# Optimization experiments

Hardware: AMD Instinct MI355X
Metric: run time of the kernel (lower is better)

Reference implementation:

```python
import jax, jax.numpy as jnp
import numpy as np


def setup_inputs() -> dict:
    key = jax.random.key(0)
    kq, kk, kv = jax.random.split(key, 3)
    S, D = 8192, 128
    return {
        "Q": jax.random.normal(kq, (S, D), dtype=jnp.float32),
        "K": jax.random.normal(kk, (S, D), dtype=jnp.float32),
        "V": jax.random.normal(kv, (S, D), dtype=jnp.float32),
    }


def reference(Q, K, V):
    d_k = Q.shape[-1]
    scale = 1.0 / jnp.sqrt(jnp.asarray(d_k, Q.dtype))
    scores = (Q @ K.T) * scale          # [S, S]
    attn = jax.nn.softmax(scores, axis=-1)
    return attn @ V                     # [S, Dv]
```

## Files before the change

### kernel.cpp

```cpp
#include <hip/hip_runtime.h>
#include <hip/hip_bf16.h>
#include <hip/hip_fp16.h>
#include <math.h>

typedef __attribute__((ext_vector_type(8))) short short8;
typedef __attribute__((ext_vector_type(16))) float f32x16;
typedef __attribute__((ext_vector_type(4))) unsigned short ushort4v;
typedef __attribute__((ext_vector_type(4))) unsigned int uint4v;

#define S 8192
#define D 128
#define QBLK 128
#define KVB 32

__device__ __forceinline__ unsigned short f2bf(float f) {
    unsigned int x = __float_as_uint(f);
    unsigned int r = x + 0x7fffu + ((x >> 16) & 1u);
    return (unsigned short)(r >> 16);
}

__device__ __forceinline__ unsigned int cvtpk(float a, float b) {
    unsigned int r;
    asm("v_cvt_pk_bf16_f32 %0, %1, %2" : "=v"(r) : "v"(a), "v"(b));
    return r;
}

__device__ __forceinline__ float fexp2(float x) { return __builtin_amdgcn_exp2f(x); }

__device__ __forceinline__ void gl_lds16(const unsigned short* g, unsigned short* l) {
    __builtin_amdgcn_global_load_lds(
        (const __attribute__((address_space(1))) unsigned int*)g,
        (__attribute__((address_space(3))) unsigned int*)l, 16, 0, 0);
}

__device__ __forceinline__ void plswap(unsigned int& a, unsigned int& b, int hi) {
#if __has_builtin(__builtin_amdgcn_permlane32_swap)
    auto r = __builtin_amdgcn_permlane32_swap((int)a, (int)b, false, false);
    a = (unsigned int)r[0];
    b = (unsigned int)r[1];
#else
    unsigned int xa = (unsigned int)__shfl_xor((int)a, 32, 64);
    unsigned int xb = (unsigned int)__shfl_xor((int)b, 32, 64);
    unsigned int na = hi ? xb : a;
    unsigned int nb = hi ? b : xa;
    a = na; b = nb;
#endif
}

union W4 { unsigned int u[4]; short8 v; };

__global__ __launch_bounds__(256) void prep_kv(const float* __restrict__ K,
                                               const float* __restrict__ V,
                                               unsigned short* __restrict__ Kb,
                                               unsigned short* __restrict__ Vt) {
    __shared__ unsigned short T[64][72];
    const float scale = 0.12751743022854459f;
    int s0 = blockIdx.x * 64, d0 = blockIdx.y * 64;
    int tr = threadIdx.x >> 4, tc = (threadIdx.x & 15) * 4;
#pragma unroll
    for (int p = 0; p < 4; ++p) {
        int r = p * 16 + tr;
        float4 kf = *reinterpret_cast<const float4*>(K + (size_t)(s0 + r) * D + d0 + tc);
        ushort4v ko = { f2bf(kf.x * scale), f2bf(kf.y * scale),
                        f2bf(kf.z * scale), f2bf(kf.w * scale) };
        *reinterpret_cast<ushort4v*>(Kb + (size_t)(s0 + r) * D + d0 + tc) = ko;
        float4 v = *reinterpret_cast<const float4*>(V + (size_t)(s0 + r) * D + d0 + tc);
        ushort4v vo = { f2bf(v.x), f2bf(v.y), f2bf(v.z), f2bf(v.w) };
        *reinterpret_cast<ushort4v*>(&T[r][tc]) = vo;
    }
    __syncthreads();
#pragma unroll
    for (int p = 0; p < 4; ++p) {
        int dr = p * 16 + tr;
        ushort4v o = { T[tc + 0][dr], T[tc + 1][dr], T[tc + 2][dr], T[tc + 3][dr] };
        *reinterpret_cast<ushort4v*>(Vt + (size_t)(d0 + dr) * S + s0 + tc) = o;
    }
}

#define QKOP(acc, kc) (acc) = __builtin_amdgcn_mfma_f32_32x32x16_bf16(              \
    *reinterpret_cast<const short8*>(                                               \
        &Kl[(size_t)c31 * 128 + (((2 * (kc) + hi) ^ (c31 & 15)) * 8)]),             \
    qf[kc], (acc), 0, 0, 0)

#define PVOP(oo, pp, dt, off) (oo) = __builtin_amdgcn_mfma_f32_32x32x16_bf16(       \
    (pp).v,                                                                          \
    *reinterpret_cast<const short8*>(                                               \
        &Vl[((dt) * 32 + c31) * 32 + ((((off) + hi) ^ sw) * 8)]),                    \
    (oo), 0, 0, 0)

#define SMEXG(g)                                                                     \
    {                                                                                \
        float e0 = fexp2(sa[4 * (g) + 0] + sb[4 * (g) + 0]);                         \
        float e1 = fexp2(sa[4 * (g) + 1] + sb[4 * (g) + 1]);                         \
        float e2 = fexp2(sa[4 * (g) + 2] + sb[4 * (g) + 2]);                         \
        float e3 = fexp2(sa[4 * (g) + 3] + sb[4 * (g) + 3]);                         \
        l_r += (e0 + e1) + (e2 + e3);                                                \
        wd[2 * (g) + 0] = cvtpk(e0, e1);                                             \
        wd[2 * (g) + 1] = cvtpk(e2, e3);                                             \
    }

#define SMFIN(PD0, PD1)                                                              \
    {                                                                                \
        plswap(wd[0], wd[2], hi); plswap(wd[1], wd[3], hi);                          \
        plswap(wd[4], wd[6], hi); plswap(wd[5], wd[7], hi);                          \
        PD0.u[0] = wd[0]; PD0.u[1] = wd[1]; PD0.u[2] = wd[2]; PD0.u[3] = wd[3];      \
        PD1.u[0] = wd[4]; PD1.u[1] = wd[5]; PD1.u[2] = wd[6]; PD1.u[3] = wd[7];      \
    }

#define STAGE_K(RING) do {                                                           \
    gl_lds16(kg[0], &Klds[RING][(w * 2 + 0) * 512]); kg[0] += (size_t)KVB * D;       \
    gl_lds16(kg[1], &Klds[RING][(w * 2 + 1) * 512]); kg[1] += (size_t)KVB * D;       \
} while (0)

#define STAGE_V(RING) do {                                                           \
    gl_lds16(vg[0], &Vlds[RING][(w * 2 + 0) * 512]); vg[0] += KVB;                   \
    gl_lds16(vg[1], &Vlds[RING][(w * 2 + 1) * 512]); vg[1] += KVB;                   \
} while (0)

#define PHASE_BARRIER() do {                                                         \
    asm volatile("s_waitcnt vmcnt(0)" ::: "memory");                                 \
    __builtin_amdgcn_s_barrier();                                                    \
    __builtin_amdgcn_sched_barrier(0);                                               \
} while (0)

#define SUBTILE(KR, VR, PP0, PP1, QQ0, QQ1)                                          \
    {                                                                                \
        const unsigned short* Kl = Klds[KR];                                         \
        const unsigned short* Vl = Vlds[VR];                                         \
        f32x16 sa, sb;                                                               \
        _Pragma("unroll")                                                            \
        for (int i = 0; i < 16; ++i) { sa[i] = 0.f; sb[i] = 0.f; }                   \
        __builtin_amdgcn_s_setprio(1);                                               \
        QKOP(sa, 0); QKOP(sb, 1); QKOP(sa, 2); QKOP(sb, 3);                          \
        QKOP(sa, 4); QKOP(sb, 5); QKOP(sa, 6); QKOP(sb, 7);                          \
        __builtin_amdgcn_s_setprio(0);                                               \
        unsigned int wd[8];                                                          \
        PVOP(o0, PP0, 0, 0); PVOP(o0, PP1, 0, 2);                                    \
        SMEXG(0);                                                                    \
        PVOP(o1, PP0, 1, 0); PVOP(o1, PP1, 1, 2);                                    \
        SMEXG(1);                                                                    \
        PVOP(o2, PP0, 2, 0); PVOP(o2, PP1, 2, 2);                                    \
        SMEXG(2);                                                                    \
        PVOP(o3, PP0, 3, 0); PVOP(o3, PP1, 3, 2);                                    \
        SMEXG(3);                                                                    \
        SMFIN(QQ0, QQ1);                                                             \
    }

#define SUBTILE_NOPV(KR, QQ0, QQ1)                                                   \
    {                                                                                \
        const unsigned short* Kl = Klds[KR];                                         \
        f32x16 sa, sb;                                                               \
        _Pragma("unroll")                                                            \
        for (int i = 0; i < 16; ++i) { sa[i] = 0.f; sb[i] = 0.f; }                   \
        __builtin_amdgcn_s_setprio(1);                                               \
        QKOP(sa, 0); QKOP(sb, 1); QKOP(sa, 2); QKOP(sb, 3);                          \
        QKOP(sa, 4); QKOP(sb, 5); QKOP(sa, 6); QKOP(sb, 7);                          \
        __builtin_amdgcn_s_setprio(0);                                               \
        unsigned int wd[8];                                                          \
        SMEXG(0); SMEXG(1); SMEXG(2); SMEXG(3);                                      \
        SMFIN(QQ0, QQ1);                                                             \
    }

__global__ __launch_bounds__(256, 2) void attn_fwd(
    const float* __restrict__ Q, const unsigned short* __restrict__ Kb,
    const unsigned short* __restrict__ Vtg, float* __restrict__ out,
    __half* __restrict__ wsO, float* __restrict__ wsL, int split)
{
    __shared__ __attribute__((aligned(16))) unsigned short Klds[4][KVB * D];
    __shared__ __attribute__((aligned(16))) unsigned short Vlds[4][D * KVB];

    const int tid  = threadIdx.x;
    const int w    = tid >> 6;
    const int lane = tid & 63;
    const int hi   = lane >> 5;
    const int c31  = lane & 31;
    const int sw   = (c31 >> 1) & 3;
    const int bid  = blockIdx.x;
    const int sp   = bid % split;
    const int qb   = bid / split;
    const int chunk  = S / split;
    const int kv0    = sp * chunk;
    const int ntiles = chunk / KVB;

    short8 qf[8];
    {
        const float* qrow = Q + (size_t)(qb * QBLK + w * 32 + c31) * D;
#pragma unroll
        for (int kc = 0; kc < 8; ++kc) {
            float4 x = *reinterpret_cast<const float4*>(qrow + kc * 16 + hi * 8);
            float4 y = *reinterpret_cast<const float4*>(qrow + kc * 16 + hi * 8 + 4);
            W4 u;
            u.u[0] = cvtpk(x.x, x.y); u.u[1] = cvtpk(x.z, x.w);
            u.u[2] = cvtpk(y.x, y.y); u.u[3] = cvtpk(y.z, y.w);
            qf[kc] = u.v;
        }
    }

    const unsigned short* kg[2];
    const unsigned short* vg[2];
#pragma unroll
    for (int i = 0; i < 2; ++i) {
        int krow = w * 8 + i * 4 + (lane >> 4);
        int kch  = (lane & 15) ^ (krow & 15);
        kg[i] = Kb + (size_t)(kv0 + krow) * D + kch * 8;
        int vrow = w * 32 + i * 16 + (lane >> 2);
        int vch  = (lane & 3) ^ ((vrow >> 1) & 3);
        vg[i] = Vtg + (size_t)vrow * S + kv0 + vch * 8;
    }

    f32x16 o0, o1, o2, o3;
#pragma unroll
    for (int i = 0; i < 16; ++i) { o0[i] = 0.f; o1[i] = 0.f; o2[i] = 0.f; o3[i] = 0.f; }
    float l_r = 0.f;
    W4 pX0, pX1, pY0, pY1;

    STAGE_K(0); STAGE_K(1); STAGE_V(0);

    PHASE_BARRIER();
    STAGE_K(2); STAGE_K(3);
    STAGE_V(1); STAGE_V(2);
    SUBTILE_NOPV(0, pY0, pY1);
    SUBTILE(1, 0, pY0, pY1, pX0, pX1);

    const int npair = ntiles / 4 - 1;
#pragma unroll 1
    for (int j = 0; j < npair; ++j) {
        PHASE_BARRIER();
        STAGE_K(0); STAGE_K(1);
        STAGE_V(3); STAGE_V(0);
        SUBTILE(2, 1, pX0, pX1, pY0, pY1);
        SUBTILE(3, 2, pY0, pY1, pX0, pX1);
        PHASE_BARRIER();
        STAGE_K(2); STAGE_K(3);
        STAGE_V(1); STAGE_V(2);
        SUBTILE(0, 3, pX0, pX1, pY0, pY1);
        SUBTILE(1, 0, pY0, pY1, pX0, pX1);
    }

    PHASE_BARRIER();
    STAGE_V(3);
    SUBTILE(2, 1, pX0, pX1, pY0, pY1);
    SUBTILE(3, 2, pY0, pY1, pX0, pX1);

    PHASE_BARRIER();
    {
        const unsigned short* Vl = Vlds[3];
        __builtin_amdgcn_s_setprio(1);
        PVOP(o0, pX0, 0, 0); PVOP(o0, pX1, 0, 2);
        PVOP(o1, pX0, 1, 0); PVOP(o1, pX1, 1, 2);
        PVOP(o2, pX0, 2, 0); PVOP(o2, pX1, 2, 2);
        PVOP(o3, pX0, 3, 0); PVOP(o3, pX1, 3, 2);
        __builtin_amdgcn_s_setprio(0);
    }

    float l_tot = l_r + __shfl_xor(l_r, 32, 64);
    if (split == 1) {
#pragma unroll
        for (int reg = 0; reg < 16; ++reg) {
            int crow = (reg & 3) + 8 * (reg >> 2) + 4 * hi;
            float lr  = __shfl(l_tot, crow, 64);
            float inv = 1.f / lr;
            size_t rb = (size_t)(qb * QBLK + w * 32 + crow) * D;
            out[rb +  0 + c31] = o0[reg] * inv;
            out[rb + 32 + c31] = o1[reg] * inv;
            out[rb + 64 + c31] = o2[reg] * inv;
            out[rb + 96 + c31] = o3[reg] * inv;
        }
    } else {
        __half* Opart = wsO + (size_t)(qb * split + sp) * (QBLK * D);
#pragma unroll
        for (int reg = 0; reg < 16; ++reg) {
            int crow = (reg & 3) + 8 * (reg >> 2) + 4 * hi;
            size_t rb = (size_t)(w * 32 + crow) * D;
            Opart[rb +  0 + c31] = __float2half(o0[reg]);
            Opart[rb + 32 + c31] = __float2half(o1[reg]);
            Opart[rb + 64 + c31] = __float2half(o2[reg]);
            Opart[rb + 96 + c31] = __float2half(o3[reg]);
        }
        if (hi == 0)
            wsL[(size_t)(qb * split + sp) * QBLK + w * 32 + c31] = l_tot;
    }
}

__global__ void attn_combine(const __half* __restrict__ wsO,
                             const float* __restrict__ wsL,
                             float* __restrict__ out, int split)
{
    int idx = blockIdx.x * blockDim.x + threadIdx.x;
    if (idx >= S * D / 8) return;
    int row = idx >> 4;
    int g   = (idx & 15) * 8;
    int qb = row >> 7, rloc = row & 127;
    float acc[8];
#pragma unroll
    for (int i = 0; i < 8; ++i) acc[i] = 0.f;
    float L = 0.f;
    for (int s = 0; s < split; ++s) {
        size_t b = (size_t)(qb * split + s);
        const __half* p = wsO + b * (QBLK * D) + (size_t)rloc * D + g;
        uint4v u = *reinterpret_cast<const uint4v*>(p);
#pragma unroll
        for (int i = 0; i < 4; ++i) {
            unsigned int wbits = u[i];
            __half2 h = *reinterpret_cast<__half2*>(&wbits);
            float2 f = __half22float2(h);
            acc[2 * i]     += f.x;
            acc[2 * i + 1] += f.y;
        }
        L += wsL[b * QBLK + rloc];
    }
    float inv = 1.f / L;
    size_t ob = (size_t)row * D + g;
    float4 w0 = { acc[0] * inv, acc[1] * inv, acc[2] * inv, acc[3] * inv };
    float4 w1 = { acc[4] * inv, acc[5] * inv, acc[6] * inv, acc[7] * inv };
    *reinterpret_cast<float4*>(out + ob)     = w0;
    *reinterpret_cast<float4*>(out + ob + 4) = w1;
}

extern "C" void kernel_launch(void* const* d_in, const int* in_sizes, int n_in,
                              void* d_out, int out_size, void* d_ws, size_t ws_size,
                              hipStream_t stream) {
    const float* Q = (const float*)d_in[0];
    const float* K = (const float*)d_in[1];
    const float* V = (const float*)d_in[2];
    float* out = (float*)d_out;

    size_t base = 2ull * S * D * sizeof(unsigned short);
    int split = 1;
    for (int sp = 8; sp >= 2; sp >>= 1) {
        size_t need = base + (size_t)sp * S * D * sizeof(__half)
                    + (size_t)sp * S * sizeof(float);
        if (ws_size >= need) { split = sp; break; }
    }

    unsigned short* Kb = (unsigned short*)d_ws;
    unsigned short* Vt = Kb + (size_t)S * D;
    __half* wsO = (__half*)(Vt + (size_t)S * D);
    float* wsL = (float*)(wsO + (size_t)split * S * D);

    prep_kv<<<dim3(S / 64, D / 64), 256, 0, stream>>>(K, V, Kb, Vt);
    attn_fwd<<<(S / QBLK) * split, 256, 0, stream>>>(Q, Kb, Vt, out, wsO, wsL, split);
    if (split > 1)
        attn_combine<<<(S * D / 8 + 255) / 256, 256, 0, stream>>>(wsO, wsL, out, split);
}
```

Before: 56.86 us.

## Pre-swizzle V into MFMA fragment layout and load it directly to registers

The prep kernel now writes V into a layout that matches the MFMA B-operand fragment order. The attention kernel loads each tile's V fragments straight from global memory into registers, which removes the V shared-memory ring, its staging and its LDS reads. The QK accumulation is merged into a single accumulator instead of two interleaved ones. The allowed split count rises to 16. This cuts LDS traffic and LDS footprint, which may help occupancy, but it exposes global-load latency inside the loop and adds register pressure from holding eight V fragments.

```diff
diff --git a/kernel.cpp b/kernel.cpp
--- a/kernel.cpp
+++ b/kernel.cpp
@@ -52,7 +52,7 @@
 __global__ __launch_bounds__(256) void prep_kv(const float* __restrict__ K,
                                                const float* __restrict__ V,
                                                unsigned short* __restrict__ Kb,
-                                               unsigned short* __restrict__ Vt) {
+                                               unsigned short* __restrict__ Vf) {
     __shared__ unsigned short T[64][72];
     const float scale = 0.12751743022854459f;
     int s0 = blockIdx.x * 64, d0 = blockIdx.y * 64;
@@ -72,8 +72,16 @@
 #pragma unroll
     for (int p = 0; p < 4; ++p) {
         int dr = p * 16 + tr;
+        int d  = d0 + dr;
+        int s  = s0 + tc;
+        int t  = s >> 5;
+        int ks = (s >> 3) & 3;
+        int dt = d >> 5;
+        int lane2 = (d & 31) | ((ks & 1) << 5);
+        int f = dt * 2 + (ks >> 1);
+        size_t idx = (((size_t)t * 8 + f) * 64 + lane2) * 8 + (s & 7);
         ushort4v o = { T[tc + 0][dr], T[tc + 1][dr], T[tc + 2][dr], T[tc + 3][dr] };
-        *reinterpret_cast<ushort4v*>(Vt + (size_t)(d0 + dr) * S + s0 + tc) = o;
+        *reinterpret_cast<ushort4v*>(Vf + idx) = o;
     }
 }
 
@@ -82,18 +90,22 @@
         &Kl[(size_t)c31 * 128 + (((2 * (kc) + hi) ^ (c31 & 15)) * 8)]),             \
     qf[kc], (acc), 0, 0, 0)
 
-#define PVOP(oo, pp, dt, off) (oo) = __builtin_amdgcn_mfma_f32_32x32x16_bf16(       \
-    (pp).v,                                                                          \
-    *reinterpret_cast<const short8*>(                                               \
-        &Vl[((dt) * 32 + c31) * 32 + ((((off) + hi) ^ sw) * 8)]),                    \
-    (oo), 0, 0, 0)
+#define PVOPR(oo, pp, dt, off) (oo) = __builtin_amdgcn_mfma_f32_32x32x16_bf16(      \
+    (pp).v, vr[(dt) * 2 + (off) / 2], (oo), 0, 0, 0)
+
+#define LOADV do {                                                                   \
+    _Pragma("unroll")                                                                \
+    for (int f_ = 0; f_ < 8; ++f_)                                                   \
+        vr[f_] = *reinterpret_cast<const short8*>(vfp + f_ * 512);                   \
+    vfp += 4096;                                                                     \
+} while (0)
 
 #define SMEXG(g)                                                                     \
     {                                                                                \
-        float e0 = fexp2(sa[4 * (g) + 0] + sb[4 * (g) + 0]);                         \
-        float e1 = fexp2(sa[4 * (g) + 1] + sb[4 * (g) + 1]);                         \
-        float e2 = fexp2(sa[4 * (g) + 2] + sb[4 * (g) + 2]);                         \
-        float e3 = fexp2(sa[4 * (g) + 3] + sb[4 * (g) + 3]);                         \
+        float e0 = fexp2(s[4 * (g) + 0]);                                            \
+        float e1 = fexp2(s[4 * (g) + 1]);                                            \
+        float e2 = fexp2(s[4 * (g) + 2]);                                            \
+        float e3 = fexp2(s[4 * (g) + 3]);                                            \
         l_r += (e0 + e1) + (e2 + e3);                                                \
         wd[2 * (g) + 0] = cvtpk(e0, e1);                                             \
         wd[2 * (g) + 1] = cvtpk(e2, e3);                                             \
@@ -112,50 +124,42 @@
     gl_lds16(kg[1], &Klds[RING][(w * 2 + 1) * 512]); kg[1] += (size_t)KVB * D;       \
 } while (0)
 
-#define STAGE_V(RING) do {                                                           \
-    gl_lds16(vg[0], &Vlds[RING][(w * 2 + 0) * 512]); vg[0] += KVB;                   \
-    gl_lds16(vg[1], &Vlds[RING][(w * 2 + 1) * 512]); vg[1] += KVB;                   \
-} while (0)
-
 #define PHASE_BARRIER() do {                                                         \
     asm volatile("s_waitcnt vmcnt(0)" ::: "memory");                                 \
     __builtin_amdgcn_s_barrier();                                                    \
     __builtin_amdgcn_sched_barrier(0);                                               \
 } while (0)
 
-#define SUBTILE(KR, VR, PP0, PP1, QQ0, QQ1)                                          \
+#define SUBTILE(KR, PP0, PP1, QQ0, QQ1)                                              \
     {                                                                                \
         const unsigned short* Kl = Klds[KR];                                         \
-        const unsigned short* Vl = Vlds[VR];                                         \
-        f32x16 sa, sb;                                                               \
+        f32x16 s;                                                                    \
         _Pragma("unroll")                                                            \
-        for (int i = 0; i < 16; ++i) { sa[i] = 0.f; sb[i] = 0.f; }                   \
+        for (int i = 0; i < 16; ++i) s[i] = 0.f;                                     \
         __builtin_amdgcn_s_setprio(1);                                               \
-        QKOP(sa, 0); QKOP(sb, 1); QKOP(sa, 2); QKOP(sb, 3);                          \
-        QKOP(sa, 4); QKOP(sb, 5); QKOP(sa, 6); QKOP(sb, 7);                          \
+        QKOP(s, 0); QKOP(s, 1); QKOP(s, 2); QKOP(s, 3);                              \
+        QKOP(s, 4); QKOP(s, 5); QKOP(s, 6); QKOP(s, 7);                              \
         __builtin_amdgcn_s_setprio(0);                                               \
         unsigned int wd[8];                                                          \
-        PVOP(o0, PP0, 0, 0); PVOP(o0, PP1, 0, 2);                                    \
-        SMEXG(0);                                                                    \
-        PVOP(o1, PP0, 1, 0); PVOP(o1, PP1, 1, 2);                                    \
-        SMEXG(1);                                                                    \
-        PVOP(o2, PP0, 2, 0); PVOP(o2, PP1, 2, 2);                                    \
-        SMEXG(2);                                                                    \
-        PVOP(o3, PP0, 3, 0); PVOP(o3, PP1, 3, 2);                                    \
-        SMEXG(3);                                                                    \
+        PVOPR(o0, PP0, 0, 0); PVOPR(o0, PP1, 0, 2); SMEXG(0);                        \
+        PVOPR(o1, PP0, 1, 0); PVOPR(o1, PP1, 1, 2); SMEXG(1);                        \
+        PVOPR(o2, PP0, 2, 0); PVOPR(o2, PP1, 2, 2); SMEXG(2);                        \
+        PVOPR(o3, PP0, 3, 0); PVOPR(o3, PP1, 3, 2); SMEXG(3);                        \
+        LOADV;                                                                       \
         SMFIN(QQ0, QQ1);                                                             \
     }
 
 #define SUBTILE_NOPV(KR, QQ0, QQ1)                                                   \
     {                                                                                \
         const unsigned short* Kl = Klds[KR];                                         \
-        f32x16 sa, sb;                                                               \
+        f32x16 s;                                                                    \
         _Pragma("unroll")                                                            \
-        for (int i = 0; i < 16; ++i) { sa[i] = 0.f; sb[i] = 0.f; }                   \
+        for (int i = 0; i < 16; ++i) s[i] = 0.f;                                     \
         __builtin_amdgcn_s_setprio(1);                                               \
-        QKOP(sa, 0); QKOP(sb, 1); QKOP(sa, 2); QKOP(sb, 3);                          \
-        QKOP(sa, 4); QKOP(sb, 5); QKOP(sa, 6); QKOP(sb, 7);                          \
+        QKOP(s, 0); QKOP(s, 1); QKOP(s, 2); QKOP(s, 3);                              \
+        QKOP(s, 4); QKOP(s, 5); QKOP(s, 6); QKOP(s, 7);                              \
         __builtin_amdgcn_s_setprio(0);                                               \
+        LOADV;                                                                       \
         unsigned int wd[8];                                                          \
         SMEXG(0); SMEXG(1); SMEXG(2); SMEXG(3);                                      \
         SMFIN(QQ0, QQ1);                                                             \
@@ -163,18 +167,16 @@
 
 __global__ __launch_bounds__(256, 2) void attn_fwd(
     const float* __restrict__ Q, const unsigned short* __restrict__ Kb,
-    const unsigned short* __restrict__ Vtg, float* __restrict__ out,
+    const unsigned short* __restrict__ Vf, float* __restrict__ out,
     __half* __restrict__ wsO, float* __restrict__ wsL, int split)
 {
     __shared__ __attribute__((aligned(16))) unsigned short Klds[4][KVB * D];
-    __shared__ __attribute__((aligned(16))) unsigned short Vlds[4][D * KVB];
 
     const int tid  = threadIdx.x;
     const int w    = tid >> 6;
     const int lane = tid & 63;
     const int hi   = lane >> 5;
     const int c31  = lane & 31;
-    const int sw   = (c31 >> 1) & 3;
     const int bid  = blockIdx.x;
     const int sp   = bid % split;
     const int qb   = bid / split;
@@ -197,16 +199,15 @@
     }
 
     const unsigned short* kg[2];
-    const unsigned short* vg[2];
 #pragma unroll
     for (int i = 0; i < 2; ++i) {
         int krow = w * 8 + i * 4 + (lane >> 4);
         int kch  = (lane & 15) ^ (krow & 15);
         kg[i] = Kb + (size_t)(kv0 + krow) * D + kch * 8;
-        int vrow = w * 32 + i * 16 + (lane >> 2);
-        int vch  = (lane & 3) ^ ((vrow >> 1) & 3);
-        vg[i] = Vtg + (size_t)vrow * S + kv0 + vch * 8;
-    }
+    }
+
+    const unsigned short* vfp = Vf + (size_t)(kv0 >> 5) * 4096 + (size_t)lane * 8;
+    short8 vr[8];
 
     f32x16 o0, o1, o2, o3;
 #pragma unroll
@@ -214,42 +215,36 @@
     float l_r = 0.f;
     W4 pX0, pX1, pY0, pY1;
 
-    STAGE_K(0); STAGE_K(1); STAGE_V(0);
+    STAGE_K(0); STAGE_K(1);
 
     PHASE_BARRIER();
     STAGE_K(2); STAGE_K(3);
-    STAGE_V(1); STAGE_V(2);
     SUBTILE_NOPV(0, pY0, pY1);
-    SUBTILE(1, 0, pY0, pY1, pX0, pX1);
+    SUBTILE(1, pY0, pY1, pX0, pX1);
 
     const int npair = ntiles / 4 - 1;
 #pragma unroll 1
     for (int j = 0; j < npair; ++j) {
         PHASE_BARRIER();
         STAGE_K(0); STAGE_K(1);
-        STAGE_V(3); STAGE_V(0);
-        SUBTILE(2, 1, pX0, pX1, pY0, pY1);
-        SUBTILE(3, 2, pY0, pY1, pX0, pX1);
+        SUBTILE(2, pX0, pX1, pY0, pY1);
+        SUBTILE(3, pY0, pY1, pX0, pX1);
         PHASE_BARRIER();
         STAGE_K(2); STAGE_K(3);
-        STAGE_V(1); STAGE_V(2);
-        SUBTILE(0, 3, pX0, pX1, pY0, pY1);
-        SUBTILE(1, 0, pY0, pY1, pX0, pX1);
+        SUBTILE(0, pX0, pX1, pY0, pY1);
+        SUBTILE(1, pY0, pY1, pX0, pX1);
     }
 
     PHASE_BARRIER();
-    STAGE_V(3);
-    SUBTILE(2, 1, pX0, pX1, pY0, pY1);
-    SUBTILE(3, 2, pY0, pY1, pX0, pX1);
-
-    PHASE_BARRIER();
+    SUBTILE(2, pX0, pX1, pY0, pY1);
+    SUBTILE(3, pY0, pY1, pX0, pX1);
+
     {
-        const unsigned short* Vl = Vlds[3];
         __builtin_amdgcn_s_setprio(1);
-        PVOP(o0, pX0, 0, 0); PVOP(o0, pX1, 0, 2);
-        PVOP(o1, pX0, 1, 0); PVOP(o1, pX1, 1, 2);
-        PVOP(o2, pX0, 2, 0); PVOP(o2, pX1, 2, 2);
-        PVOP(o3, pX0, 3, 0); PVOP(o3, pX1, 3, 2);
+        PVOPR(o0, pX0, 0, 0); PVOPR(o0, pX1, 0, 2);
+        PVOPR(o1, pX0, 1, 0); PVOPR(o1, pX1, 1, 2);
+        PVOPR(o2, pX0, 2, 0); PVOPR(o2, pX1, 2, 2);
+        PVOPR(o3, pX0, 3, 0); PVOPR(o3, pX1, 3, 2);
         __builtin_amdgcn_s_setprio(0);
     }
 
@@ -327,19 +322,19 @@
 
     size_t base = 2ull * S * D * sizeof(unsigned short);
     int split = 1;
-    for (int sp = 8; sp >= 2; sp >>= 1) {
+    for (int sp = 16; sp >= 2; sp >>= 1) {
         size_t need = base + (size_t)sp * S * D * sizeof(__half)
                     + (size_t)sp * S * sizeof(float);
         if (ws_size >= need) { split = sp; break; }
     }
 
     unsigned short* Kb = (unsigned short*)d_ws;
-    unsigned short* Vt = Kb + (size_t)S * D;
-    __half* wsO = (__half*)(Vt + (size_t)S * D);
+    unsigned short* Vf = Kb + (size_t)S * D;
+    __half* wsO = (__half*)(Vf + (size_t)S * D);
     float* wsL = (float*)(wsO + (size_t)split * S * D);
 
-    prep_kv<<<dim3(S / 64, D / 64), 256, 0, stream>>>(K, V, Kb, Vt);
-    attn_fwd<<<(S / QBLK) * split, 256, 0, stream>>>(Q, Kb, Vt, out, wsO, wsL, split);
+    prep_kv<<<dim3(S / 64, D / 64), 256, 0, stream>>>(K, V, Kb, Vf);
+    attn_fwd<<<(S / QBLK) * split, 256, 0, stream>>>(Q, Kb, Vf, out, wsO, wsL, split);
     if (split > 1)
         attn_combine<<<(S * D / 8 + 255) / 256, 256, 0, stream>>>(wsO, wsL, out, split);
 }
```

Result: slower. 61.43 us (+8.0%).

## Shrink LDS ring to three slots with mid-phase barrier and allow split 16

Applied to the files above, without the earlier changes.

Replaces the four-slot K/V LDS ring with a three-slot rotating ring, adding a mid-phase barrier so each subtile stages only one K and one V tile ahead. This cuts LDS use per block, which may let more blocks fit per CU. The KV split factor cap also rises from 8 to 16, giving more parallel blocks at the cost of a heavier combine pass and more workspace traffic. The extra barrier adds synchronisation per subtile.

```diff
diff --git a/kernel.cpp b/kernel.cpp
--- a/kernel.cpp
+++ b/kernel.cpp
@@ -12,6 +12,7 @@
 #define D 128
 #define QBLK 128
 #define KVB 32
+#define RING (KVB * D)
 
 __device__ __forceinline__ unsigned short f2bf(float f) {
     unsigned int x = __float_as_uint(f);
@@ -107,14 +108,16 @@
         PD1.u[0] = wd[4]; PD1.u[1] = wd[5]; PD1.u[2] = wd[6]; PD1.u[3] = wd[7];      \
     }
 
-#define STAGE_K(RING) do {                                                           \
-    gl_lds16(kg[0], &Klds[RING][(w * 2 + 0) * 512]); kg[0] += (size_t)KVB * D;       \
-    gl_lds16(kg[1], &Klds[RING][(w * 2 + 1) * 512]); kg[1] += (size_t)KVB * D;       \
+#define STAGE_K(R) do {                                                              \
+    unsigned short* kd = Klds + (size_t)(R) * RING;                                  \
+    gl_lds16(kg[0], kd + (w * 2 + 0) * 512); kg[0] += (size_t)KVB * D;               \
+    gl_lds16(kg[1], kd + (w * 2 + 1) * 512); kg[1] += (size_t)KVB * D;               \
 } while (0)
 
-#define STAGE_V(RING) do {                                                           \
-    gl_lds16(vg[0], &Vlds[RING][(w * 2 + 0) * 512]); vg[0] += KVB;                   \
-    gl_lds16(vg[1], &Vlds[RING][(w * 2 + 1) * 512]); vg[1] += KVB;                   \
+#define STAGE_V(R) do {                                                              \
+    unsigned short* vd = Vlds + (size_t)(R) * RING;                                  \
+    gl_lds16(vg[0], vd + (w * 2 + 0) * 512); vg[0] += KVB;                           \
+    gl_lds16(vg[1], vd + (w * 2 + 1) * 512); vg[1] += KVB;                           \
 } while (0)
 
 #define PHASE_BARRIER() do {                                                         \
@@ -123,10 +126,16 @@
     __builtin_amdgcn_sched_barrier(0);                                               \
 } while (0)
 
-#define SUBTILE(KR, VR, PP0, PP1, QQ0, QQ1)                                          \
+#define MID_BARRIER() do {                                                           \
+    __builtin_amdgcn_sched_barrier(0);                                               \
+    __builtin_amdgcn_s_barrier();                                                    \
+    __builtin_amdgcn_sched_barrier(0);                                               \
+} while (0)
+
+#define SUBTILE(KL, VL, PP0, PP1, QQ0, QQ1)                                          \
     {                                                                                \
-        const unsigned short* Kl = Klds[KR];                                         \
-        const unsigned short* Vl = Vlds[VR];                                         \
+        const unsigned short* Kl = (KL);                                             \
+        const unsigned short* Vl = (VL);                                             \
         f32x16 sa, sb;                                                               \
         _Pragma("unroll")                                                            \
         for (int i = 0; i < 16; ++i) { sa[i] = 0.f; sb[i] = 0.f; }                   \
@@ -146,9 +155,9 @@
         SMFIN(QQ0, QQ1);                                                             \
     }
 
-#define SUBTILE_NOPV(KR, QQ0, QQ1)                                                   \
+#define SUBTILE_NOPV(KL, QQ0, QQ1)                                                   \
     {                                                                                \
-        const unsigned short* Kl = Klds[KR];                                         \
+        const unsigned short* Kl = (KL);                                             \
         f32x16 sa, sb;                                                               \
         _Pragma("unroll")                                                            \
         for (int i = 0; i < 16; ++i) { sa[i] = 0.f; sb[i] = 0.f; }                   \
@@ -166,8 +175,8 @@
     const unsigned short* __restrict__ Vtg, float* __restrict__ out,
     __half* __restrict__ wsO, float* __restrict__ wsL, int split)
 {
-    __shared__ __attribute__((aligned(16))) unsigned short Klds[4][KVB * D];
-    __shared__ __attribute__((aligned(16))) unsigned short Vlds[4][D * KVB];
+    __shared__ __attribute__((aligned(16))) unsigned short Klds[3 * RING];
+    __shared__ __attribute__((aligned(16))) unsigned short Vlds[3 * RING];
 
     const int tid  = threadIdx.x;
     const int w    = tid >> 6;
@@ -181,6 +190,7 @@
     const int chunk  = S / split;
     const int kv0    = sp * chunk;
     const int ntiles = chunk / KVB;
+    const int P      = ntiles / 2;
 
     short8 qf[8];
     {
@@ -214,37 +224,48 @@
     float l_r = 0.f;
     W4 pX0, pX1, pY0, pY1;
 
+    int r0 = 0, r1 = 1, r2 = 2;
+
     STAGE_K(0); STAGE_K(1); STAGE_V(0);
 
     PHASE_BARRIER();
-    STAGE_K(2); STAGE_K(3);
-    STAGE_V(1); STAGE_V(2);
-    SUBTILE_NOPV(0, pY0, pY1);
-    SUBTILE(1, 0, pY0, pY1, pX0, pX1);
-
-    const int npair = ntiles / 4 - 1;
+    STAGE_K(2);
+    STAGE_V(1);
+    SUBTILE_NOPV(Klds + (size_t)r0 * RING, pY0, pY1);
+    MID_BARRIER();
+    STAGE_K(0);
+    STAGE_V(2);
+    SUBTILE(Klds + (size_t)r1 * RING, Vlds + (size_t)r0 * RING,
+            pY0, pY1, pX0, pX1);
+
 #pragma unroll 1
-    for (int j = 0; j < npair; ++j) {
+    for (int p = 1; p <= P - 2; ++p) {
+        int t = r2; r2 = r1; r1 = r0; r0 = t;
         PHASE_BARRIER();
-        STAGE_K(0); STAGE_K(1);
-        STAGE_V(3); STAGE_V(0);
-        SUBTILE(2, 1, pX0, pX1, pY0, pY1);
-        SUBTILE(3, 2, pY0, pY1, pX0, pX1);
+        STAGE_K(r2);
+        STAGE_V(r1);
+        SUBTILE(Klds + (size_t)r0 * RING, Vlds + (size_t)r2 * RING,
+                pX0, pX1, pY0, pY1);
+        MID_BARRIER();
+        STAGE_K(r0);
+        STAGE_V(r2);
+        SUBTILE(Klds + (size_t)r1 * RING, Vlds + (size_t)r0 * RING,
+                pY0, pY1, pX0, pX1);
+    }
+
+    {
+        int t = r2; r2 = r1; r1 = r0; r0 = t;
         PHASE_BARRIER();
-        STAGE_K(2); STAGE_K(3);
-        STAGE_V(1); STAGE_V(2);
-        SUBTILE(0, 3, pX0, pX1, pY0, pY1);
-        SUBTILE(1, 0, pY0, pY1, pX0, pX1);
-    }
-
-    PHASE_BARRIER();
-    STAGE_V(3);
-    SUBTILE(2, 1, pX0, pX1, pY0, pY1);
-    SUBTILE(3, 2, pY0, pY1, pX0, pX1);
+        STAGE_V(r1);
+        SUBTILE(Klds + (size_t)r0 * RING, Vlds + (size_t)r2 * RING,
+                pX0, pX1, pY0, pY1);
+        SUBTILE(Klds + (size_t)r1 * RING, Vlds + (size_t)r0 * RING,
+                pY0, pY1, pX0, pX1);
+    }
 
     PHASE_BARRIER();
     {
-        const unsigned short* Vl = Vlds[3];
+        const unsigned short* Vl = Vlds + (size_t)r1 * RING;
         __builtin_amdgcn_s_setprio(1);
         PVOP(o0, pX0, 0, 0); PVOP(o0, pX1, 0, 2);
         PVOP(o1, pX0, 1, 0); PVOP(o1, pX1, 1, 2);
@@ -327,7 +348,7 @@
 
     size_t base = 2ull * S * D * sizeof(unsigned short);
     int split = 1;
-    for (int sp = 8; sp >= 2; sp >>= 1) {
+    for (int sp = 16; sp >= 2; sp >>= 1) {
         size_t need = base + (size_t)sp * S * D * sizeof(__half)
                     + (size_t)sp * S * sizeof(float);
         if (ws_size >= need) { split = sp; break; }
```

Result: slower. 65.51 us (+15.2%).
